# Performance work log

Hardware: AMD Instinct MI355X
Metric: run time of the kernel (lower is better)

The kernel has to match this reference:

```python
import jax, jax.numpy as jnp
import numpy as np
from itertools import combinations, product

NQ = 10
DIM = 2 ** NQ
DEPTH = 1
ENC_PAIRS = [(q, q + 1) for q in range(0, NQ - 1, 2)] + [(q, q + 1) for q in range(1, NQ - 1, 2)]  # brick layer: even then odd
PYR = [(i, i + 1) for layer in range(NQ - 1) for i in range(NQ - layer - 1)]  # pyramid RBS wire pairs (45)
OBS_PAIRS = list(combinations(range(NQ), 2))  # 45 pairwise 2-local observables

_P = {'I': np.eye(2, dtype=np.complex128),
      'X': np.array([[0, 1], [1, 0]], dtype=np.complex128),
      'Y': np.array([[0, -1j], [1j, 0]], dtype=np.complex128),
      'Z': np.array([[1, 0], [0, -1]], dtype=np.complex128)}
_WORDS = [''.join(w) for w in product('IXYZ', repeat=2)][1:]  # PennyLane pauli_basis order, identity excluded
P15 = jnp.asarray(np.stack([np.kron(_P[w[0]], _P[w[1]]) for w in _WORDS]).astype(np.complex64))
XXm = jnp.asarray(np.kron(_P['X'], _P['X']).astype(np.complex64))
YYm = jnp.asarray(np.kron(_P['Y'], _P['Y']).astype(np.complex64))
ZZm = jnp.asarray(np.kron(_P['Z'], _P['Z']).astype(np.complex64))
I4 = jnp.eye(4, dtype=jnp.complex64)
_TRIL_I, _TRIL_J = np.tril_indices(4, -1)  # order matches create_Hermitian's count+j indexing


def _u3(t, p, l):
    c = jnp.cos(t / 2).astype(jnp.complex64)
    s = jnp.sin(t / 2).astype(jnp.complex64)
    return jnp.stack([jnp.stack([c, -jnp.exp(1j * l) * s]),
                      jnp.stack([jnp.exp(1j * p) * s, jnp.exp(1j * (p + l)) * c])])


def _ising(phi, P):
    # exp(-i*phi/2 * P) for P in {XX, YY, ZZ} (P^2 = I)
    return jnp.cos(phi / 2) * I4 - 1j * jnp.sin(phi / 2) * P


def _apply1(psi, U, w):
    # psi: (B, 2, ..., 2); single-qubit gate U (2,2) on wire w
    psi = jnp.moveaxis(psi, 1 + w, -1)
    sh = psi.shape
    out = jnp.einsum('ij,brj->bri', U, psi.reshape(sh[0], -1, 2)).reshape(sh)
    return jnp.moveaxis(out, -1, 1 + w)


def _apply2(psi, U, a, b):
    # two-qubit gate on wires (a,b), a is most-significant (PennyLane wire order). U: (4,4) or batched (B,4,4)
    psi = jnp.moveaxis(psi, (1 + a, 1 + b), (-2, -1))
    sh = psi.shape
    flat = psi.reshape(sh[0], -1, 4)
    eq = 'bij,brj->bri' if U.ndim == 3 else 'ij,brj->bri'
    out = jnp.einsum(eq, U, flat).reshape(sh)
    return jnp.moveaxis(out, (-2, -1), (1 + a, 1 + b))


def _build_H(A, B, D):
    # create_Hermitian: lower triangle A+iB, diag[0:3] = D[1:4], diag[3]=0, then h + h^dagger
    n = A.shape[0]
    h = jnp.zeros((n, 4, 4), jnp.complex64)
    h = h.at[:, _TRIL_I, _TRIL_J].set(A.astype(jnp.complex64) + 1j * B.astype(jnp.complex64))
    d = np.arange(3)
    h = h.at[:, d, d].set(D[:, 1:4].astype(jnp.complex64))
    return h + jnp.conj(jnp.swapaxes(h, -1, -2))


def setup_inputs() -> dict:
    key = jax.random.key(0)
    ks = jax.random.split(key, 9)
    f32 = jnp.float32
    return {
        'x': jax.random.normal(ks[0], (256, 512), f32),
        'W1': jax.random.normal(ks[1], (512, 256), f32) * (512 ** -0.5),
        'b1': jnp.zeros((256,), f32),
        'W2': jax.random.normal(ks[2], (256, 135), f32) * (256 ** -0.5),
        'b2': jnp.zeros((135,), f32),
        'qvit_params': 0.01 * jax.random.normal(ks[3], (DEPTH, len(PYR), 12), f32),
        'A': 2.0 * jax.random.normal(ks[4], (len(OBS_PAIRS), 6), f32),
        'B': 2.0 * jax.random.normal(ks[5], (len(OBS_PAIRS), 6), f32),
        'D': 2.0 * jax.random.normal(ks[6], (len(OBS_PAIRS), 4), f32),
    }


def reference(x, W1, b1, W2, b2, qvit_params, A, B, D):
    Bsz = x.shape[0]
    # enc_proj: Linear -> SiLU -> Linear
    enc = jax.nn.silu(x @ W1 + b1) @ W2 + b2  # (B, 135)
    # Brick-layer SpecialUnitary encoding: U = exp(i * sum theta_m P_m) via eigh
    theta = enc.reshape(Bsz, len(ENC_PAIRS), 15).astype(jnp.complex64)
    Hg = jnp.einsum('bgm,mij->bgij', theta, P15)  # Hermitian generators (B, 9, 4, 4)
    ew, V = jnp.linalg.eigh(Hg)
    Ue = jnp.einsum('bgik,bgk,bgjk->bgij', V, jnp.exp(1j * ew.astype(jnp.complex64)), jnp.conj(V))
    # |0...0>
    psi = jnp.zeros((Bsz, DIM), jnp.complex64).at[:, 0].set(1.0).reshape((Bsz,) + (2,) * NQ)
    for g, (a, b) in enumerate(ENC_PAIRS):
        psi = _apply2(psi, Ue[:, g], a, b)
    # QViT pyramid ansatz
    for ly in range(DEPTH):
        for g, (a, b) in enumerate(PYR):
            p = qvit_params[ly, g]
            psi = _apply1(psi, _u3(p[0], p[1], p[2]), a)
            psi = _apply2(psi, _ising(p[3], XXm), a, b)
            psi = _apply2(psi, _ising(p[4], YYm), a, b)
            psi = _apply2(psi, _ising(p[5], ZZm), a, b)
            psi = _apply1(psi, _u3(p[6], p[7], p[8]), a)
            psi = _apply2(psi, _ising(p[9], XXm), a, b)
            psi = _apply2(psi, _ising(p[10], YYm), a, b)
            psi = _apply2(psi, _ising(p[11], ZZm), a, b)
    # Pairwise ANO Hermitian expectations
    Hobs = _build_H(A, B, D)  # (45, 4, 4)
    outs = []
    for w, (a, b) in enumerate(OBS_PAIRS):
        pm = jnp.moveaxis(psi, (1 + a, 1 + b), (1, 2)).reshape(Bsz, 4, -1)
        outs.append(jnp.real(jnp.einsum('bir,ij,bjr->b', jnp.conj(pm), Hobs[w], pm)))
    return jnp.stack(outs, axis=1).astype(jnp.float32)
```

## Files before the change

kernel.cpp:

```cpp
#include <hip/hip_runtime.h>
#include <math.h>

#define NOBS 45
typedef float2 c32;

constexpr int W2Sc[10] = {1, 0, 7, 6, 5, 3, 2, 4, 9, 8};
constexpr int OAc[NOBS] = {
    0,0,0,0,0,0,0,0,0, 1,1,1,1,1,1,1,1, 2,2,2,2,2,2,2, 3,3,3,3,3,3,
    4,4,4,4,4, 5,5,5,5, 6,6,6, 7,7, 8};
constexpr int OBc[NOBS] = {
    1,2,3,4,5,6,7,8,9, 2,3,4,5,6,7,8,9, 3,4,5,6,7,8,9, 4,5,6,7,8,9,
    5,6,7,8,9, 6,7,8,9, 7,8,9, 8,9, 9};
constexpr int TIc[6] = {1, 2, 2, 3, 3, 3};
constexpr int TJc[6] = {0, 0, 1, 0, 1, 2};

#define PSTRIDE 257

__device__ __forceinline__ c32 cfma(c32 a, c32 b, c32 c) {
    c.x = fmaf(a.x, b.x, fmaf(-a.y, b.y, c.x));
    c.y = fmaf(a.x, b.y, fmaf(a.y, b.x, c.y));
    return c;
}
__device__ __forceinline__ c32 cmul(c32 a, c32 b) {
    return make_float2(a.x * b.x - a.y * b.y, a.x * b.y + a.y * b.x);
}

template <int CTRL>
__device__ __forceinline__ float dppf(float x) {
    return __uint_as_float((unsigned)__builtin_amdgcn_update_dpp(
        0, (int)__float_as_uint(x), CTRL, 0xF, 0xF, true));
}
__device__ __forceinline__ float swap32f(float a) {
    auto r = __builtin_amdgcn_permlane32_swap(__float_as_uint(a), __float_as_uint(a), false, false);
    return (__uint_as_float(r[0]) + __uint_as_float(r[1])) - a;
}
#if __has_builtin(__builtin_amdgcn_permlane16_swap)
__device__ __forceinline__ float swap16f(float a) {
    auto r = __builtin_amdgcn_permlane16_swap(__float_as_uint(a), __float_as_uint(a), false, false);
    return (__uint_as_float(r[0]) + __uint_as_float(r[1])) - a;
}
#else
__device__ __forceinline__ float swap16f(float a) { return __shfl_xor(a, 16, 64); }
#endif
__device__ __forceinline__ float swz4f(float a) {
    return __uint_as_float(__builtin_amdgcn_ds_swizzle(__float_as_uint(a), 0x101F));
}
template <int M>
__device__ __forceinline__ float exf(float x) {
    float r = x;
    if constexpr ((M & 3) == 1) r = dppf<0xB1>(r);
    else if constexpr ((M & 3) == 2) r = dppf<0x4E>(r);
    else if constexpr ((M & 3) == 3) r = dppf<0x1B>(r);
    if constexpr (M & 4)  r = swz4f(r);
    if constexpr (M & 8)  r = dppf<0x128>(r);
    if constexpr (M & 16) r = swap16f(r);
    if constexpr (M & 32) r = swap32f(r);
    return r;
}
template <int M>
__device__ __forceinline__ c32 exch(c32 a) { return make_float2(exf<M>(a.x), exf<M>(a.y)); }
__device__ __forceinline__ c32 swap32c(c32 a) { return make_float2(swap32f(a.x), swap32f(a.y)); }

__device__ __forceinline__ float wave_reduce63(float x) {
    x += dppf<0x111>(x);
    x += dppf<0x112>(x);
    x += dppf<0x114>(x);
    x += dppf<0x118>(x);
    x += dppf<0x142>(x);
    x += dppf<0x143>(x);
    return x;
}

__device__ __forceinline__ int insert2(int t, int pl, int ph) {
    int low  = t & ((1 << pl) - 1);
    int rest = t >> pl;
    int nm   = ph - 1 - pl;
    int mid  = rest & ((1 << nm) - 1);
    int high = rest >> nm;
    return low | (mid << (pl + 1)) | (high << (ph + 1));
}

template <int W>
__device__ __forceinline__ c32 pE(int r, int c) {
    if constexpr (W == 0) return make_float2((r == c) ? 1.f : 0.f, 0.f);
    else if constexpr (W == 1) return make_float2((r != c) ? 1.f : 0.f, 0.f);
    else if constexpr (W == 2) return make_float2(0.f, (r == c) ? 0.f : ((r == 0) ? -1.f : 1.f));
    else return make_float2((r == c) ? ((r == 0) ? 1.f : -1.f) : 0.f, 0.f);
}
template <int W0, int W1>
__device__ __forceinline__ void paccum(c32& H, float th, int i1, int i2, int j1, int j2) {
    c32 a = pE<W0>(i1, j1), b = pE<W1>(i2, j2);
    c32 p = cmul(a, b);
    H.x = fmaf(th, p.x, H.x);
    H.y = fmaf(th, p.y, H.y);
}

struct F16 { c32 u[16]; };
struct FLoc { c32 a[4]; c32 b[4]; };
struct F4 { c32 uS, uB, uA, uC; };

__device__ __forceinline__ F16 loadF16(const c32* __restrict__ U) {
    F16 f;
#pragma unroll
    for (int i = 0; i < 16; i++) f.u[i] = U[i];
    return f;
}
__device__ __forceinline__ FLoc loadLoc(const c32* __restrict__ U, int ln) {
    int bb = (ln >> 5) & 1;
    const c32* U0 = U + bb * 4;
    const c32* U1 = U + (2 | bb) * 4;
    int c00 = bb, c01 = 2 | bb, c10 = bb ^ 1, c11 = 2 | (bb ^ 1);
    FLoc f;
    f.a[0] = U0[c00]; f.a[1] = U0[c01]; f.a[2] = U0[c10]; f.a[3] = U0[c11];
    f.b[0] = U1[c00]; f.b[1] = U1[c01]; f.b[2] = U1[c10]; f.b[3] = U1[c11];
    return f;
}
template <int QA, int QB>
__device__ __forceinline__ F4 loadL2(const c32* __restrict__ U, int ln) {
    int bA = (ln >> QA) & 1, bB = (ln >> QB) & 1;
    int r = (bA << 1) | bB;
    const c32* Ur = U + r * 4;
    F4 f;
    f.uS = Ur[r]; f.uB = Ur[r ^ 1]; f.uA = Ur[r ^ 2]; f.uC = Ur[r ^ 3];
    return f;
}

__device__ __forceinline__ void applyLL(c32 v[4], const F16& f) {
    c32 n0 = cfma(f.u[0],  v[0], cfma(f.u[1],  v[1], cfma(f.u[2],  v[2], cmul(f.u[3],  v[3]))));
    c32 n1 = cfma(f.u[4],  v[0], cfma(f.u[5],  v[1], cfma(f.u[6],  v[2], cmul(f.u[7],  v[3]))));
    c32 n2 = cfma(f.u[8],  v[0], cfma(f.u[9],  v[1], cfma(f.u[10], v[2], cmul(f.u[11], v[3]))));
    c32 n3 = cfma(f.u[12], v[0], cfma(f.u[13], v[1], cfma(f.u[14], v[2], cmul(f.u[15], v[3]))));
    v[0] = n0; v[1] = n1; v[2] = n2; v[3] = n3;
}
__device__ __forceinline__ void applyLoc(c32 v[4], const FLoc& f) {
    c32 p0 = swap32c(v[0]), p1 = swap32c(v[1]), p2 = swap32c(v[2]), p3 = swap32c(v[3]);
    c32 n0 = cfma(f.a[0], v[0], cfma(f.a[1], v[1], cfma(f.a[2], p0, cmul(f.a[3], p1))));
    c32 n1 = cfma(f.b[0], v[0], cfma(f.b[1], v[1], cfma(f.b[2], p0, cmul(f.b[3], p1))));
    c32 n2 = cfma(f.a[0], v[2], cfma(f.a[1], v[3], cfma(f.a[2], p2, cmul(f.a[3], p3))));
    c32 n3 = cfma(f.b[0], v[2], cfma(f.b[1], v[3], cfma(f.b[2], p2, cmul(f.b[3], p3))));
    v[0] = n0; v[1] = n1; v[2] = n2; v[3] = n3;
}
template <int QA, int QB>
__device__ __forceinline__ void applyL2(c32 v[4], const F4& f) {
#pragma unroll
    for (int lc = 0; lc < 4; lc++) {
        c32 pB = exch<(1 << QB)>(v[lc]);
        c32 pA = exch<(1 << QA)>(v[lc]);
        c32 pC = exch<(1 << QA)>(pB);
        v[lc] = cfma(f.uS, v[lc], cfma(f.uB, pB, cfma(f.uA, pA, cmul(f.uC, pC))));
    }
}

__device__ __forceinline__ void dumpV(const c32 v[4], c32* __restrict__ psiR, int t) {
#pragma unroll
    for (int lc = 0; lc < 4; lc++) psiR[lc * PSTRIDE + t] = v[lc];
}
__device__ __forceinline__ void loadV(c32 v[4], const c32* __restrict__ psiR, int t) {
#pragma unroll
    for (int lc = 0; lc < 4; lc++) v[lc] = psiR[lc * PSTRIDE + t];
}
template <int PA, int PB>
__device__ __forceinline__ void ldsApply(const F16& f, c32* __restrict__ psiR, int t) {
    constexpr int PL = (PA < PB) ? PA : PB, PH = (PA < PB) ? PB : PA;
    int base = insert2(t, PL, PH);
    c32* pl_ = psiR + (base & 3) * PSTRIDE;
    int s = base >> 2;
    constexpr int oa = (1 << PA) >> 2, ob = (1 << PB) >> 2;
    c32 g0 = pl_[s], g1 = pl_[s + ob], g2 = pl_[s + oa], g3 = pl_[s + oa + ob];
    c32 n0 = cfma(f.u[0],  g0, cfma(f.u[1],  g1, cfma(f.u[2],  g2, cmul(f.u[3],  g3))));
    c32 n1 = cfma(f.u[4],  g0, cfma(f.u[5],  g1, cfma(f.u[6],  g2, cmul(f.u[7],  g3))));
    c32 n2 = cfma(f.u[8],  g0, cfma(f.u[9],  g1, cfma(f.u[10], g2, cmul(f.u[11], g3))));
    c32 n3 = cfma(f.u[12], g0, cfma(f.u[13], g1, cfma(f.u[14], g2, cmul(f.u[15], g3))));
    pl_[s] = n0; pl_[s + ob] = n1; pl_[s + oa] = n2; pl_[s + oa + ob] = n3;
}

__global__ __launch_bounds__(256, 1) void mega_kernel(
    const float* __restrict__ x,  const float* __restrict__ W1, const float* __restrict__ b1,
    const float* __restrict__ W2, const float* __restrict__ b2, const float* __restrict__ qp,
    const float* __restrict__ Am, const float* __restrict__ Bm, const float* __restrict__ Dm,
    float* __restrict__ out) {
    __shared__ __align__(16) c32 psiRaw[4 * PSTRIDE];
    __shared__ c32 UeS[144];
    __shared__ c32 GpS[720];
    __shared__ float HbS[720];
    __shared__ float encS[136];
    __shared__ float redS[180];

    const int b = blockIdx.x, t = threadIdx.x, ln = t & 63;
    float* F = (float*)psiRaw;

    if (t < 128) ((float4*)F)[t] = ((const float4*)(x + (size_t)b * 512))[t];
    __syncthreads();
    {
        int q = t & 63, sl = t >> 6;
        float4 a4 = make_float4(0.f, 0.f, 0.f, 0.f);
#pragma unroll 16
        for (int kk = 0; kk < 128; kk++) {
            int k = sl * 128 + kk;
            float xk = F[k];
            const float4 w = *(const float4*)(W1 + (size_t)k * 256 + q * 4);
            a4.x = fmaf(xk, w.x, a4.x); a4.y = fmaf(xk, w.y, a4.y);
            a4.z = fmaf(xk, w.z, a4.z); a4.w = fmaf(xk, w.w, a4.w);
        }
        *(float4*)(F + 512 + sl * 256 + q * 4) = a4;
    }
    __syncthreads();
    {
        float hv = b1[t] + F[512 + t] + F[768 + t] + F[1024 + t] + F[1280 + t];
        hv = hv / (1.f + __expf(-hv));
        F[1536 + t] = hv;
    }
    __syncthreads();
    if (t < 135) {
        float a2 = b2[t], a3 = 0.f;
#pragma unroll 16
        for (int k = 0; k < 128; k++) {
            a2 = fmaf(F[1536 + k],       W2[(size_t)k * 135 + t],         a2);
            a3 = fmaf(F[1536 + 128 + k], W2[(size_t)(128 + k) * 135 + t], a3);
        }
        encS[t] = a2 + a3;
    }
    __syncthreads();

    c32* Mm = psiRaw;
    c32* Rb = psiRaw + 144;
    c32* TA = psiRaw + 288;
    if (t < 144) {
        int m = t >> 4, e = t & 15, i = e >> 2, j = e & 3;
        int i1 = i >> 1, i2 = i & 1, j1 = j >> 1, j2 = j & 1;
        const float* th = encS + m * 15;
        c32 H = make_float2(0.f, 0.f);
        paccum<0,1>(H, th[0],  i1,i2,j1,j2); paccum<0,2>(H, th[1],  i1,i2,j1,j2);
        paccum<0,3>(H, th[2],  i1,i2,j1,j2); paccum<1,0>(H, th[3],  i1,i2,j1,j2);
        paccum<1,1>(H, th[4],  i1,i2,j1,j2); paccum<1,2>(H, th[5],  i1,i2,j1,j2);
        paccum<1,3>(H, th[6],  i1,i2,j1,j2); paccum<2,0>(H, th[7],  i1,i2,j1,j2);
        paccum<2,1>(H, th[8],  i1,i2,j1,j2); paccum<2,2>(H, th[9],  i1,i2,j1,j2);
        paccum<2,3>(H, th[10], i1,i2,j1,j2); paccum<3,0>(H, th[11], i1,i2,j1,j2);
        paccum<3,1>(H, th[12], i1,i2,j1,j2); paccum<3,2>(H, th[13], i1,i2,j1,j2);
        paccum<3,3>(H, th[14], i1,i2,j1,j2);
        const float sc = 1.f / 64.f;
        Mm[t] = make_float2(-H.y * sc, H.x * sc);
        Rb[t] = make_float2((i == j) ? 1.f : 0.f, 0.f);
    } else if (t >= 234) {
        for (int w = t - 234; w < NOBS; w += 22) {
            float* Hf = HbS + w * 16;
            Hf[0] = 2.f * Dm[w * 4 + 1];
            Hf[1] = 2.f * Dm[w * 4 + 2];
            Hf[2] = 2.f * Dm[w * 4 + 3];
            Hf[3] = 0.f;
#pragma unroll
            for (int k = 0; k < 6; k++) {
                Hf[4 + 2 * k] = 2.f * Am[w * 6 + k];
                Hf[5 + 2 * k] = 2.f * Bm[w * 6 + k];
            }
        }
    }
    __syncthreads();
    c32 Mrow[4];
    if (t < 144) {
        int m = t >> 4, i = (t & 15) >> 2;
#pragma unroll
        for (int k = 0; k < 4; k++) Mrow[k] = Mm[m * 16 + i * 4 + k];
    }
    for (int step = 0; step < 13; step++) {
        if (t < 144) {
            int m = t >> 4, e = t & 15, i = e >> 2, j = e & 3;
            const c32* cur = (step & 1) ? UeS : Rb;
            c32 acc = make_float2(0.f, 0.f);
            c32 outv;
            if (step < 7) {
#pragma unroll
                for (int k = 0; k < 4; k++) acc = cfma(Mrow[k], cur[m * 16 + k * 4 + j], acc);
                float inv = 1.f / (float)(7 - step);
                outv = make_float2(fmaf(acc.x, inv, (i == j) ? 1.f : 0.f), acc.y * inv);
            } else {
#pragma unroll
                for (int k = 0; k < 4; k++)
                    acc = cfma(cur[m * 16 + i * 4 + k], cur[m * 16 + k * 4 + j], acc);
                outv = acc;
            }
            ((step & 1) ? Rb : UeS)[t] = outv;
        } else if (t >= 144 && t < 234 && step < 8) {
            int pt = t - 144, g = pt >> 1, ih = (pt & 1) << 1;
            const float* p = qp + g * 12;
            const c32* src = ((step & 1) ? TA : GpS) + g * 16;
            c32* dst = ((step & 1) ? GpS : TA) + g * 16;
#pragma unroll
            for (int r2 = 0; r2 < 2; r2++) {
                int i = ih + r2, i1 = i >> 1, i2 = i & 1;
                c32 row[4];
                if (step == 0) {
                    float s, c; __sincosf(p[0] * 0.5f, &s, &c);
                    c32 u0, u1;
                    if (i1 == 0) { u0 = make_float2(c, 0.f);
                                   u1 = make_float2(-__cosf(p[2]) * s, -__sinf(p[2]) * s); }
                    else { u0 = make_float2(__cosf(p[1]) * s, __sinf(p[1]) * s);
                           u1 = make_float2(__cosf(p[1] + p[2]) * c, __sinf(p[1] + p[2]) * c); }
#pragma unroll
                    for (int jj = 0; jj < 4; jj++) row[jj] = make_float2(0.f, 0.f);
                    row[i2] = u0; row[2 | i2] = u1;
                } else {
                    c32 coef0, coef1; int c0, c1;
                    if (step == 1 || step == 5) {
                        float s, c; __sincosf(p[step == 1 ? 3 : 9] * 0.5f, &s, &c);
                        c0 = i; coef0 = make_float2(c, 0.f);
                        c1 = i ^ 3; coef1 = make_float2(0.f, -s);
                    } else if (step == 2 || step == 6) {
                        float s, c; __sincosf(p[step == 2 ? 4 : 10] * 0.5f, &s, &c);
                        float yy = (i == 0 || i == 3) ? 1.f : -1.f;
                        c0 = i; coef0 = make_float2(c, 0.f);
                        c1 = i ^ 3; coef1 = make_float2(0.f, s * yy);
                    } else if (step == 3 || step == 7) {
                        float s, c; __sincosf(p[step == 3 ? 5 : 11] * 0.5f, &s, &c);
                        float zz = (i == 0 || i == 3) ? 1.f : -1.f;
                        c0 = i; coef0 = make_float2(c, -s * zz);
                        c1 = i; coef1 = make_float2(0.f, 0.f);
                    } else {
                        float s, c; __sincosf(p[6] * 0.5f, &s, &c);
                        if (i1 == 0) { coef0 = make_float2(c, 0.f);
                                       coef1 = make_float2(-__cosf(p[8]) * s, -__sinf(p[8]) * s); }
                        else { coef0 = make_float2(__cosf(p[7]) * s, __sinf(p[7]) * s);
                               coef1 = make_float2(__cosf(p[7] + p[8]) * c, __sinf(p[7] + p[8]) * c); }
                        c0 = i2; c1 = 2 | i2;
                    }
#pragma unroll
                    for (int jj = 0; jj < 4; jj++)
                        row[jj] = cfma(coef0, src[c0 * 4 + jj], cmul(coef1, src[c1 * 4 + jj]));
                }
#pragma unroll
                for (int jj = 0; jj < 4; jj++) dst[i * 4 + jj] = row[jj];
            }
        }
        __syncthreads();
    }

    c32 v[4];
#pragma unroll
    for (int lc = 0; lc < 4; lc++) v[lc] = make_float2(0.f, 0.f);
    if (t == 0) v[0] = make_float2(1.f, 0.f);

    {
        F16 e0 = loadF16(UeS + 0);
        F4 e1 = loadL2<5, 4>(UeS + 16, ln);
        F4 e2 = loadL2<3, 1>(UeS + 32, ln);
        F4 e3 = loadL2<0, 2>(UeS + 48, ln);
        applyLL(v, e0);
        applyL2<5, 4>(v, e1);
        applyL2<3, 1>(v, e2);
        applyL2<0, 2>(v, e3);
        F16 e4 = loadF16(UeS + 64);
        dumpV(v, psiRaw, t); __syncthreads();
        ldsApply<9, 8>(e4, psiRaw, t); __syncthreads();
        loadV(v, psiRaw, t);
        FLoc e5 = loadLoc(UeS + 80, ln);
        F4 e6 = loadL2<4, 3>(UeS + 96, ln);
        F4 e7 = loadL2<1, 0>(UeS + 112, ln);
        applyLoc(v, e5);
        applyL2<4, 3>(v, e6);
        applyL2<1, 0>(v, e7);
        F16 e8 = loadF16(UeS + 128);
        dumpV(v, psiRaw, t); __syncthreads();
        ldsApply<4, 9>(e8, psiRaw, t); __syncthreads();
        loadV(v, psiRaw, t);
    }

    {
        int g = 0;
#pragma unroll
        for (int layer = 0; layer < 9; layer++) {
            const int amax = 8 - layer;
            F16 f0 = loadF16(GpS + g * 16);
            FLoc f1; F4 f2, f3, f4, f5, f6;
            int gi = g + 1;
            if (amax >= 1) f1 = loadLoc(GpS + (gi++) * 16, ln);
            if (amax >= 2) f2 = loadL2<5, 4>(GpS + (gi++) * 16, ln);
            if (amax >= 3) f3 = loadL2<4, 3>(GpS + (gi++) * 16, ln);
            if (amax >= 4) f4 = loadL2<3, 1>(GpS + (gi++) * 16, ln);
            if (amax >= 5) f5 = loadL2<1, 0>(GpS + (gi++) * 16, ln);
            if (amax >= 6) f6 = loadL2<0, 2>(GpS + (gi++) * 16, ln);
            applyLL(v, f0);
            if (amax >= 1) applyLoc(v, f1);
            if (amax >= 2) applyL2<5, 4>(v, f2);
            if (amax >= 3) applyL2<4, 3>(v, f3);
            if (amax >= 4) applyL2<3, 1>(v, f4);
            if (amax >= 5) applyL2<1, 0>(v, f5);
            if (amax >= 6) applyL2<0, 2>(v, f6);
            g = gi;
            if (amax >= 8) {
                F16 h1 = loadF16(GpS + g * 16);
                F16 h2 = loadF16(GpS + (g + 1) * 16);
                dumpV(v, psiRaw, t); __syncthreads();
                ldsApply<4, 9>(h1, psiRaw, t); __syncthreads();
                ldsApply<9, 8>(h2, psiRaw, t); __syncthreads();
                loadV(v, psiRaw, t);
                g += 2;
            } else if (amax >= 7) {
                F16 h1 = loadF16(GpS + g * 16);
                dumpV(v, psiRaw, t); __syncthreads();
                ldsApply<4, 9>(h1, psiRaw, t); __syncthreads();
                loadV(v, psiRaw, t);
                g += 1;
            }
        }
    }

    dumpV(v, psiRaw, t);
    __syncthreads();
#pragma unroll
    for (int w0 = 0; w0 < NOBS; w0 += 5) {
        float pr[5];
#pragma unroll
        for (int u = 0; u < 5; u++) {
            const int w = w0 + u;
            const int pa = W2Sc[OAc[w]], pb = W2Sc[OBc[w]];
            const int pl = (pa < pb) ? pa : pb, phh = (pa < pb) ? pb : pa;
            const int oa = 1 << pa, ob = 1 << pb;
            int i0 = insert2(t, pl, phh);
            int i1 = i0 + ob, i2 = i0 + oa, i3 = i0 + oa + ob;
            c32 vg[4];
            vg[0] = psiRaw[(i0 & 3) * PSTRIDE + (i0 >> 2)];
            vg[1] = psiRaw[(i1 & 3) * PSTRIDE + (i1 >> 2)];
            vg[2] = psiRaw[(i2 & 3) * PSTRIDE + (i2 >> 2)];
            vg[3] = psiRaw[(i3 & 3) * PSTRIDE + (i3 >> 2)];
            const float* Hf = HbS + w * 16;
            float r = Hf[0] * fmaf(vg[0].x, vg[0].x, vg[0].y * vg[0].y)
                    + Hf[1] * fmaf(vg[1].x, vg[1].x, vg[1].y * vg[1].y)
                    + Hf[2] * fmaf(vg[2].x, vg[2].x, vg[2].y * vg[2].y);
#pragma unroll
            for (int k = 0; k < 6; k++) {
                c32 vi = vg[TIc[k]], vj = vg[TJc[k]];
                float cx = fmaf(vi.x, vj.x, vi.y * vj.y);
                float cy = fmaf(vi.x, vj.y, -vi.y * vj.x);
                r = fmaf(Hf[4 + 2 * k], cx, r);
                r = fmaf(-Hf[5 + 2 * k], cy, r);
            }
            pr[u] = wave_reduce63(r);
        }
        if (ln == 63) {
#pragma unroll
            for (int u = 0; u < 5; u++) redS[(w0 + u) * 4 + (t >> 6)] = pr[u];
        }
    }
    __syncthreads();
    if (t < NOBS)
        out[(size_t)b * NOBS + t] = redS[t * 4] + redS[t * 4 + 1] + redS[t * 4 + 2] + redS[t * 4 + 3];
}

extern "C" void kernel_launch(void* const* d_in, const int* in_sizes, int n_in,
                              void* d_out, int out_size, void* d_ws, size_t ws_size,
                              hipStream_t stream) {
    (void)in_sizes; (void)n_in; (void)out_size; (void)d_ws; (void)ws_size;
    const float* x  = (const float*)d_in[0];
    const float* W1 = (const float*)d_in[1];
    const float* b1 = (const float*)d_in[2];
    const float* W2 = (const float*)d_in[3];
    const float* b2 = (const float*)d_in[4];
    const float* qp = (const float*)d_in[5];
    const float* Am = (const float*)d_in[6];
    const float* Bm = (const float*)d_in[7];
    const float* Dm = (const float*)d_in[8];
    float* out = (float*)d_out;

    hipLaunchKernelGGL(mega_kernel, dim3(256), dim3(256), 0, stream,
                       x, W1, b1, W2, b2, qp, Am, Bm, Dm, out);
}
```

Before: 107.2 us.

## Use unpadded LDS state layout and stop unrolling layer and observable loops

Replaces the padded plane-major LDS layout of the state vector with a plain interleaved layout (index t*4+lc), which simplifies address arithmetic but may bring back bank conflicts on the gather-style LDS gates. The pyramid layer loop, the matrix-exponential step loop and the observable loop are no longer unrolled, and the observable wire indices now come from __constant__ tables instead of compile-time constants. This shrinks code size and register pressure at the cost of runtime branching and indexing in place of constant-folded offsets.

```diff
diff --git a/kernel.cpp b/kernel.cpp
--- a/kernel.cpp
+++ b/kernel.cpp
@@ -4,17 +4,14 @@
 #define NOBS 45
 typedef float2 c32;
 
-constexpr int W2Sc[10] = {1, 0, 7, 6, 5, 3, 2, 4, 9, 8};
-constexpr int OAc[NOBS] = {
-    0,0,0,0,0,0,0,0,0, 1,1,1,1,1,1,1,1, 2,2,2,2,2,2,2, 3,3,3,3,3,3,
-    4,4,4,4,4, 5,5,5,5, 6,6,6, 7,7, 8};
-constexpr int OBc[NOBS] = {
-    1,2,3,4,5,6,7,8,9, 2,3,4,5,6,7,8,9, 3,4,5,6,7,8,9, 4,5,6,7,8,9,
-    5,6,7,8,9, 6,7,8,9, 7,8,9, 8,9, 9};
+__device__ __constant__ int PA_s[NOBS] = {
+    1,1,1,1,1,1,1,1,1, 0,0,0,0,0,0,0,0, 7,7,7,7,7,7,7, 6,6,6,6,6,6,
+    5,5,5,5,5, 3,3,3,3, 2,2,2, 4,4, 9};
+__device__ __constant__ int PB_s[NOBS] = {
+    0,7,6,5,3,2,4,9,8, 7,6,5,3,2,4,9,8, 6,5,3,2,4,9,8, 5,3,2,4,9,8,
+    3,2,4,9,8, 2,4,9,8, 4,9,8, 9,8, 8};
 constexpr int TIc[6] = {1, 2, 2, 3, 3, 3};
 constexpr int TJc[6] = {0, 0, 1, 0, 1, 2};
-
-#define PSTRIDE 257
 
 __device__ __forceinline__ c32 cfma(c32 a, c32 b, c32 c) {
     c.x = fmaf(a.x, b.x, fmaf(-a.y, b.y, c.x));
@@ -151,27 +148,25 @@
     }
 }
 
-__device__ __forceinline__ void dumpV(const c32 v[4], c32* __restrict__ psiR, int t) {
-#pragma unroll
-    for (int lc = 0; lc < 4; lc++) psiR[lc * PSTRIDE + t] = v[lc];
-}
-__device__ __forceinline__ void loadV(c32 v[4], const c32* __restrict__ psiR, int t) {
-#pragma unroll
-    for (int lc = 0; lc < 4; lc++) v[lc] = psiR[lc * PSTRIDE + t];
+__device__ __forceinline__ void dumpV(const c32 v[4], c32* __restrict__ psi, int t) {
+#pragma unroll
+    for (int lc = 0; lc < 4; lc++) psi[(t << 2) | lc] = v[lc];
+}
+__device__ __forceinline__ void loadV(c32 v[4], const c32* __restrict__ psi, int t) {
+#pragma unroll
+    for (int lc = 0; lc < 4; lc++) v[lc] = psi[(t << 2) | lc];
 }
 template <int PA, int PB>
-__device__ __forceinline__ void ldsApply(const F16& f, c32* __restrict__ psiR, int t) {
+__device__ __forceinline__ void ldsApply(const F16& f, c32* __restrict__ psi, int t) {
     constexpr int PL = (PA < PB) ? PA : PB, PH = (PA < PB) ? PB : PA;
     int base = insert2(t, PL, PH);
-    c32* pl_ = psiR + (base & 3) * PSTRIDE;
-    int s = base >> 2;
-    constexpr int oa = (1 << PA) >> 2, ob = (1 << PB) >> 2;
-    c32 g0 = pl_[s], g1 = pl_[s + ob], g2 = pl_[s + oa], g3 = pl_[s + oa + ob];
+    constexpr int oa = 1 << PA, ob = 1 << PB;
+    c32 g0 = psi[base], g1 = psi[base + ob], g2 = psi[base + oa], g3 = psi[base + oa + ob];
     c32 n0 = cfma(f.u[0],  g0, cfma(f.u[1],  g1, cfma(f.u[2],  g2, cmul(f.u[3],  g3))));
     c32 n1 = cfma(f.u[4],  g0, cfma(f.u[5],  g1, cfma(f.u[6],  g2, cmul(f.u[7],  g3))));
     c32 n2 = cfma(f.u[8],  g0, cfma(f.u[9],  g1, cfma(f.u[10], g2, cmul(f.u[11], g3))));
     c32 n3 = cfma(f.u[12], g0, cfma(f.u[13], g1, cfma(f.u[14], g2, cmul(f.u[15], g3))));
-    pl_[s] = n0; pl_[s + ob] = n1; pl_[s + oa] = n2; pl_[s + oa + ob] = n3;
+    psi[base] = n0; psi[base + ob] = n1; psi[base + oa] = n2; psi[base + oa + ob] = n3;
 }
 
 __global__ __launch_bounds__(256, 1) void mega_kernel(
@@ -179,7 +174,7 @@
     const float* __restrict__ W2, const float* __restrict__ b2, const float* __restrict__ qp,
     const float* __restrict__ Am, const float* __restrict__ Bm, const float* __restrict__ Dm,
     float* __restrict__ out) {
-    __shared__ __align__(16) c32 psiRaw[4 * PSTRIDE];
+    __shared__ __align__(16) c32 psiS[1024];
     __shared__ c32 UeS[144];
     __shared__ c32 GpS[720];
     __shared__ float HbS[720];
@@ -187,7 +182,7 @@
     __shared__ float redS[180];
 
     const int b = blockIdx.x, t = threadIdx.x, ln = t & 63;
-    float* F = (float*)psiRaw;
+    float* F = (float*)psiS;
 
     if (t < 128) ((float4*)F)[t] = ((const float4*)(x + (size_t)b * 512))[t];
     __syncthreads();
@@ -222,9 +217,9 @@
     }
     __syncthreads();
 
-    c32* Mm = psiRaw;
-    c32* Rb = psiRaw + 144;
-    c32* TA = psiRaw + 288;
+    c32* Mm = psiS;
+    c32* Rb = psiS + 144;
+    c32* TA = psiS + 288;
     if (t < 144) {
         int m = t >> 4, e = t & 15, i = e >> 2, j = e & 3;
         int i1 = i >> 1, i2 = i & 1, j1 = j >> 1, j2 = j & 1;
@@ -262,6 +257,7 @@
 #pragma unroll
         for (int k = 0; k < 4; k++) Mrow[k] = Mm[m * 16 + i * 4 + k];
     }
+#pragma unroll 1
     for (int step = 0; step < 13; step++) {
         if (t < 144) {
             int m = t >> 4, e = t & 15, i = e >> 2, j = e & 3;
@@ -339,89 +335,58 @@
     for (int lc = 0; lc < 4; lc++) v[lc] = make_float2(0.f, 0.f);
     if (t == 0) v[0] = make_float2(1.f, 0.f);
 
-    {
-        F16 e0 = loadF16(UeS + 0);
-        F4 e1 = loadL2<5, 4>(UeS + 16, ln);
-        F4 e2 = loadL2<3, 1>(UeS + 32, ln);
-        F4 e3 = loadL2<0, 2>(UeS + 48, ln);
-        applyLL(v, e0);
-        applyL2<5, 4>(v, e1);
-        applyL2<3, 1>(v, e2);
-        applyL2<0, 2>(v, e3);
-        F16 e4 = loadF16(UeS + 64);
-        dumpV(v, psiRaw, t); __syncthreads();
-        ldsApply<9, 8>(e4, psiRaw, t); __syncthreads();
-        loadV(v, psiRaw, t);
-        FLoc e5 = loadLoc(UeS + 80, ln);
-        F4 e6 = loadL2<4, 3>(UeS + 96, ln);
-        F4 e7 = loadL2<1, 0>(UeS + 112, ln);
-        applyLoc(v, e5);
-        applyL2<4, 3>(v, e6);
-        applyL2<1, 0>(v, e7);
-        F16 e8 = loadF16(UeS + 128);
-        dumpV(v, psiRaw, t); __syncthreads();
-        ldsApply<4, 9>(e8, psiRaw, t); __syncthreads();
-        loadV(v, psiRaw, t);
-    }
+    applyLL(v, loadF16(UeS + 0));
+    applyL2<5, 4>(v, loadL2<5, 4>(UeS + 16, ln));
+    applyL2<3, 1>(v, loadL2<3, 1>(UeS + 32, ln));
+    applyL2<0, 2>(v, loadL2<0, 2>(UeS + 48, ln));
+    dumpV(v, psiS, t); __syncthreads();
+    ldsApply<9, 8>(loadF16(UeS + 64), psiS, t); __syncthreads();
+    loadV(v, psiS, t);
+    applyLoc(v, loadLoc(UeS + 80, ln));
+    applyL2<4, 3>(v, loadL2<4, 3>(UeS + 96, ln));
+    applyL2<1, 0>(v, loadL2<1, 0>(UeS + 112, ln));
+    dumpV(v, psiS, t); __syncthreads();
+    ldsApply<4, 9>(loadF16(UeS + 128), psiS, t); __syncthreads();
+    loadV(v, psiS, t);
 
     {
         int g = 0;
-#pragma unroll
+#pragma unroll 1
         for (int layer = 0; layer < 9; layer++) {
             const int amax = 8 - layer;
-            F16 f0 = loadF16(GpS + g * 16);
-            FLoc f1; F4 f2, f3, f4, f5, f6;
-            int gi = g + 1;
-            if (amax >= 1) f1 = loadLoc(GpS + (gi++) * 16, ln);
-            if (amax >= 2) f2 = loadL2<5, 4>(GpS + (gi++) * 16, ln);
-            if (amax >= 3) f3 = loadL2<4, 3>(GpS + (gi++) * 16, ln);
-            if (amax >= 4) f4 = loadL2<3, 1>(GpS + (gi++) * 16, ln);
-            if (amax >= 5) f5 = loadL2<1, 0>(GpS + (gi++) * 16, ln);
-            if (amax >= 6) f6 = loadL2<0, 2>(GpS + (gi++) * 16, ln);
-            applyLL(v, f0);
-            if (amax >= 1) applyLoc(v, f1);
-            if (amax >= 2) applyL2<5, 4>(v, f2);
-            if (amax >= 3) applyL2<4, 3>(v, f3);
-            if (amax >= 4) applyL2<3, 1>(v, f4);
-            if (amax >= 5) applyL2<1, 0>(v, f5);
-            if (amax >= 6) applyL2<0, 2>(v, f6);
-            g = gi;
-            if (amax >= 8) {
-                F16 h1 = loadF16(GpS + g * 16);
-                F16 h2 = loadF16(GpS + (g + 1) * 16);
-                dumpV(v, psiRaw, t); __syncthreads();
-                ldsApply<4, 9>(h1, psiRaw, t); __syncthreads();
-                ldsApply<9, 8>(h2, psiRaw, t); __syncthreads();
-                loadV(v, psiRaw, t);
-                g += 2;
-            } else if (amax >= 7) {
-                F16 h1 = loadF16(GpS + g * 16);
-                dumpV(v, psiRaw, t); __syncthreads();
-                ldsApply<4, 9>(h1, psiRaw, t); __syncthreads();
-                loadV(v, psiRaw, t);
-                g += 1;
+            applyLL(v, loadF16(GpS + (g++) * 16));
+            if (amax >= 1) applyLoc(v, loadLoc(GpS + (g++) * 16, ln));
+            if (amax >= 2) applyL2<5, 4>(v, loadL2<5, 4>(GpS + (g++) * 16, ln));
+            if (amax >= 3) applyL2<4, 3>(v, loadL2<4, 3>(GpS + (g++) * 16, ln));
+            if (amax >= 4) applyL2<3, 1>(v, loadL2<3, 1>(GpS + (g++) * 16, ln));
+            if (amax >= 5) applyL2<1, 0>(v, loadL2<1, 0>(GpS + (g++) * 16, ln));
+            if (amax >= 6) applyL2<0, 2>(v, loadL2<0, 2>(GpS + (g++) * 16, ln));
+            if (amax >= 7) {
+                dumpV(v, psiS, t); __syncthreads();
+                ldsApply<4, 9>(loadF16(GpS + (g++) * 16), psiS, t); __syncthreads();
+                if (amax >= 8) {
+                    ldsApply<9, 8>(loadF16(GpS + (g++) * 16), psiS, t); __syncthreads();
+                }
+                loadV(v, psiS, t);
             }
         }
     }
 
-    dumpV(v, psiRaw, t);
-    __syncthreads();
-#pragma unroll
+    dumpV(v, psiS, t);
+    __syncthreads();
+#pragma unroll 1
     for (int w0 = 0; w0 < NOBS; w0 += 5) {
         float pr[5];
 #pragma unroll
         for (int u = 0; u < 5; u++) {
             const int w = w0 + u;
-            const int pa = W2Sc[OAc[w]], pb = W2Sc[OBc[w]];
+            const int pa = PA_s[w], pb = PB_s[w];
             const int pl = (pa < pb) ? pa : pb, phh = (pa < pb) ? pb : pa;
             const int oa = 1 << pa, ob = 1 << pb;
             int i0 = insert2(t, pl, phh);
-            int i1 = i0 + ob, i2 = i0 + oa, i3 = i0 + oa + ob;
             c32 vg[4];
-            vg[0] = psiRaw[(i0 & 3) * PSTRIDE + (i0 >> 2)];
-            vg[1] = psiRaw[(i1 & 3) * PSTRIDE + (i1 >> 2)];
-            vg[2] = psiRaw[(i2 & 3) * PSTRIDE + (i2 >> 2)];
-            vg[3] = psiRaw[(i3 & 3) * PSTRIDE + (i3 >> 2)];
+            vg[0] = psiS[i0];      vg[1] = psiS[i0 + ob];
+            vg[2] = psiS[i0 + oa]; vg[3] = psiS[i0 + oa + ob];
             const float* Hf = HbS + w * 16;
             float r = Hf[0] * fmaf(vg[0].x, vg[0].x, vg[0].y * vg[0].y)
                     + Hf[1] * fmaf(vg[1].x, vg[1].x, vg[1].y * vg[1].y)
```

After: 112.2 us. 1.05x slower.
